# Kernel optimization log

Hardware: AMD Instinct MI355X
Metric: run time of the kernel (lower is better)

The kernel has to match this reference:

```python
import jax, jax.numpy as jnp
import numpy as np

B, NMAX, T, FIN, H, K, OUT = 64, 256, 16, 3, 32, 8, 64
N = B * NMAX            # 16384 total nodes
EPG = 2048              # edges per graph
E = B * EPG             # 131072 edges
EPS = 1e-15


def gcn_conv(x, src, dst, ew, W, b):
    # x: [N, T, FIN] -> [N, T, H]; GCNConv: symmetric norm with self-loops (weight 1)
    xw = jnp.einsum('ntf,fh->nth', x, W)
    loops = jnp.arange(N, dtype=src.dtype)
    src_a = jnp.concatenate([src, loops])
    dst_a = jnp.concatenate([dst, loops])
    w_a = jnp.concatenate([ew, jnp.ones((N,), ew.dtype)])
    deg = jax.ops.segment_sum(w_a, dst_a, num_segments=N)
    dinv = jnp.where(deg > 0, jax.lax.rsqrt(deg), 0.0)
    norm = dinv[src_a] * w_a * dinv[dst_a]
    out = jax.ops.segment_sum(xw[src_a] * norm[:, None, None], dst_a, num_segments=N)
    return out + b


def dense_mincut_pool(x, adj, s):
    # x [B,T,Nc,H], adj [B,Nc,Nc], s [B,Nc,Kc]  (mask is all-True: equal-size graphs)
    s = jax.nn.softmax(s, axis=-1)
    kc = s.shape[-1]
    out = jnp.einsum('bnk,btnh->btkh', s, x)
    out_adj = jnp.einsum('bnk,bnm,bml->bkl', s, adj, s)
    mincut_num = jnp.trace(out_adj, axis1=-2, axis2=-1)
    d_flat = adj.sum(-1)
    mincut_den = jnp.einsum('bnk,bn,bnk->b', s, d_flat, s)
    mincut_loss = -jnp.mean(mincut_num / mincut_den)
    ss = jnp.einsum('bnk,bnl->bkl', s, s)
    i_s = jnp.eye(kc, dtype=x.dtype)
    ss_n = jnp.linalg.norm(ss, axis=(-2, -1), keepdims=True)
    ortho_loss = jnp.mean(jnp.linalg.norm(ss / ss_n - i_s / jnp.sqrt(kc), axis=(-2, -1)))
    out_adj = out_adj * (1.0 - i_s)  # zero diagonal
    d = jnp.sqrt(out_adj.sum(-1))[:, None, :] + EPS  # [B,1,K]
    out_adj = out_adj / d / jnp.swapaxes(d, 1, 2)
    return out, out_adj, mincut_loss, ortho_loss


def dense_graph_conv(x, adj, Wrel, brel, Wroot):
    # DenseGraphConv(aggr='add'): lin_rel(adj @ x) + lin_root(x)
    agg = jnp.einsum('bnm,btmh->btnh', adj, x)
    return jnp.einsum('btnh,ho->btno', agg, Wrel) + brel + jnp.einsum('btnh,ho->btno', x, Wroot)


def _forward(pos, edge_attr, W1, b1, Wp1, bp1, Wrel2, brel2, Wroot2, Wp2, bp2,
             Wrel3, brel3, Wroot3, Wp3, bp3, Wrel4, brel4, Wroot4, edge_src, edge_dst):
    x = jax.nn.relu(gcn_conv(pos, edge_src, edge_dst, edge_attr, W1, b1))  # [N,T,H]
    # to_dense_batch (equal-size graphs => reshape) then transpose(1,2)
    xd = x.reshape(B, NMAX, T, H).transpose(0, 2, 1, 3)  # [B,T,NMAX,H]
    gb = edge_src // NMAX
    adj = jnp.zeros((B, NMAX, NMAX), jnp.float32).at[gb, edge_src % NMAX, edge_dst % NMAX].add(1.0)
    s1 = jnp.tanh((jnp.einsum('btnh,hk->btnk', xd, Wp1) + bp1).mean(1))   # [B,NMAX,8K]
    x1, adj1, mc1, o1 = dense_mincut_pool(xd, adj, s1)
    x1 = dense_graph_conv(x1, adj1, Wrel2, brel2, Wroot2)
    s2 = jnp.tanh((jnp.einsum('btnh,hk->btnk', x1, Wp2) + bp2).mean(1))   # [B,8K,4K]
    x2, adj2, mc2, o2 = dense_mincut_pool(x1, adj1, s2)
    x2 = dense_graph_conv(x2, adj2, Wrel3, brel3, Wroot3)
    s3 = jnp.tanh((jnp.einsum('btnh,hk->btnk', x2, Wp3) + bp3).mean(1))   # [B,4K,K]
    x3, adj3, mc3, o3 = dense_mincut_pool(x2, adj2, s3)
    x3 = dense_graph_conv(x3, adj3, Wrel4, brel4, Wroot4)                 # [B,T,K,OUT]
    p1 = jax.nn.softmax(s1, -1)
    p2 = jax.nn.softmax(s2, -1)
    p3 = jax.nn.softmax(s3, -1)
    agg = jnp.einsum('bnk,bkl,blm->bnm', p1, p2, p3)                       # [B,NMAX,K]
    return x3, mc1 + mc2 + mc3, o1 + o2 + o3, agg


def setup_inputs():
    key = jax.random.key(0)
    ks = jax.random.split(key, 16)
    pos = jax.random.normal(ks[0], (N, T, FIN), jnp.float32)
    gid = jnp.repeat(jnp.arange(B, dtype=jnp.int32), EPG)
    sl = jax.random.randint(ks[1], (E,), 0, NMAX, jnp.int32)
    dl = jax.random.randint(ks[2], (E,), 0, NMAX, jnp.int32)
    edge_src = gid * NMAX + sl
    edge_dst = gid * NMAX + dl
    edge_attr = jax.random.uniform(ks[3], (E,), jnp.float32)

    def lin(k, i, o):
        return jax.random.normal(k, (i, o), jnp.float32) / np.sqrt(i)

    return dict(
        pos=pos, edge_attr=edge_attr, edge_src=edge_src, edge_dst=edge_dst,
        W1=lin(ks[4], FIN, H), b1=jnp.zeros((H,), jnp.float32),
        Wp1=lin(ks[5], H, 8 * K), bp1=jnp.zeros((8 * K,), jnp.float32),
        Wrel2=lin(ks[6], H, H), brel2=jnp.zeros((H,), jnp.float32), Wroot2=lin(ks[7], H, H),
        Wp2=lin(ks[8], H, 4 * K), bp2=jnp.zeros((4 * K,), jnp.float32),
        Wrel3=lin(ks[9], H, H), brel3=jnp.zeros((H,), jnp.float32), Wroot3=lin(ks[10], H, H),
        Wp3=lin(ks[11], H, K), bp3=jnp.zeros((K,), jnp.float32),
        Wrel4=lin(ks[12], H, OUT), brel4=jnp.zeros((OUT,), jnp.float32), Wroot4=lin(ks[13], H, OUT),
    )


def reference(pos, edge_attr, edge_src, edge_dst, W1, b1, Wp1, bp1, Wrel2, brel2, Wroot2,
              Wp2, bp2, Wrel3, brel3, Wroot3, Wp3, bp3, Wrel4, brel4, Wroot4):
    return _forward(pos, edge_attr, W1, b1, Wp1, bp1, Wrel2, brel2, Wroot2, Wp2, bp2,
                    Wrel3, brel3, Wroot3, Wp3, bp3, Wrel4, brel4, Wroot4, edge_src, edge_dst)
```

## Files before the change

kernel.cpp:

```cpp
#include <hip/hip_runtime.h>
#include <math.h>

#define NB 64
#define TC 16
#define HC 32
#define NNODES 16384
#define NEDGES 131072
#define EPG 2048
#define EPSV 1e-15f

static inline int GRID(int n) { return (n + 255) / 256; }

template<int V> struct Log2 { static constexpr int v = 1 + Log2<V/2>::v; };
template<> struct Log2<1> { static constexpr int v = 0; };

__device__ inline float blk_sum256(float v, float* rbuf) {
    for (int o = 32; o > 0; o >>= 1) v += __shfl_xor(v, o);
    __syncthreads();
    if ((threadIdx.x & 63) == 0) rbuf[threadIdx.x >> 6] = v;
    __syncthreads();
    return rbuf[0] + rbuf[1] + rbuf[2] + rbuf[3];
}

__device__ inline float blk_sum512(float v, float* rbuf) {
    for (int o = 32; o > 0; o >>= 1) v += __shfl_xor(v, o);
    __syncthreads();
    if ((threadIdx.x & 63) == 0) rbuf[threadIdx.x >> 6] = v;
    __syncthreads();
    float s = 0.f;
#pragma unroll
    for (int i = 0; i < 8; ++i) s += rbuf[i];
    return s;
}

__global__ __launch_bounds__(256) void k_front(
        const int* __restrict__ esrc, const int* __restrict__ edst,
        const float* __restrict__ ea, const float* __restrict__ pos,
        const float* __restrict__ W1, const float* __restrict__ b1,
        const float* __restrict__ Wp1, const float* __restrict__ bp1,
        float* __restrict__ z, float* __restrict__ dinv_g,
        float* __restrict__ p1, float* __restrict__ mc) {
    __shared__ float L[9280];
    float* dinvs = L;
    float* as_   = L + 256;
    float* bs    = L + 1408;
    float* s1    = L + 256;
    float* zs    = L + 2944;
    float* poss  = L + 4480;
    float* xm    = L + 6016;
    float* wp    = L + 7040;
    float* W1s   = L + 9088;
    float* b1s   = L + 9184;
    float* bp1s  = L + 9216;
    int bid = blockIdx.x;
    int b = (bid & 7) * 8 + (bid >> 6);
    int dtile = ((bid >> 3) & 7) * 32;
    int tid = threadIdx.x;
    if (bid == 0 && tid < 2) mc[tid] = 0.f;
    for (int i = tid; i < 512; i += 256) ((float4*)wp)[i] = ((const float4*)Wp1)[i];
    if (tid < 96) W1s[tid] = W1[tid];
    if (tid < 32) b1s[tid] = b1[tid];
    if (tid < 64) bp1s[tid] = bp1[tid];
    for (int i = tid; i < 384; i += 256)
        ((float4*)poss)[i] = ((const float4*)(pos + ((size_t)b * 256 + dtile) * 48))[i];
    int ebase = b * EPG;
    int svr[8], dvr[8];
    float evr[8];
#pragma unroll
    for (int j = 0; j < 8; ++j) {
        int e = ebase + tid + j * 256;
        svr[j] = esrc[e] & 255;
        dvr[j] = edst[e] & 255;
        evr[j] = ea[e];
    }
    dinvs[tid] = 1.0f;
    __syncthreads();
#pragma unroll
    for (int j = 0; j < 8; ++j) atomicAdd(&dinvs[dvr[j]], evr[j]);
    __syncthreads();
    float dg = dinvs[tid];
    float dvv = (dg > 0.f) ? rsqrtf(dg) : 0.f;
    __syncthreads();
    dinvs[tid] = dvv;
    __syncthreads();
    if (dtile == 0) dinv_g[b * 256 + tid] = dinvs[tid];
    int d = tid >> 3, q = tid & 7;
    float acc[6];
#pragma unroll
    for (int j = 0; j < 6; ++j) acc[j] = 0.f;
    const float* pbase = pos + (size_t)b * 256 * 48;
    for (int s0 = 0; s0 < 256; s0 += 32) {
        for (int i = tid; i < 288; i += 256)
            ((float4*)as_)[i] = make_float4(0.f, 0.f, 0.f, 0.f);
        __syncthreads();
#pragma unroll
        for (int j = 0; j < 8; ++j) {
            int dr = dvr[j] - dtile, sc = svr[j] - s0;
            if ((unsigned)dr < 32u && (unsigned)sc < 32u)
                atomicAdd(&as_[dr * 36 + sc], evr[j]);
        }
        for (int i = tid; i < 384; i += 256) {
            int r = i / 12, c = i % 12;
            float4 v = *(const float4*)(pbase + (size_t)(s0 + r) * 48 + c * 4);
            float dd = dinvs[s0 + r];
            v.x *= dd; v.y *= dd; v.z *= dd; v.w *= dd;
            *(float4*)(bs + r * 48 + c * 4) = v;
        }
        __syncthreads();
#pragma unroll 8
        for (int sp = 0; sp < 32; ++sp) {
            float a = as_[d * 36 + sp];
            const float* bp = &bs[sp * 48 + q * 6];
#pragma unroll
            for (int j = 0; j < 6; ++j) acc[j] += a * bp[j];
        }
        __syncthreads();
    }
    float dd = dinvs[dtile + d];
    float* zr = z + (size_t)(b * 256 + dtile + d) * 48 + q * 6;
#pragma unroll
    for (int j = 0; j < 6; ++j) {
        float v = acc[j] * dd;
        zr[j] = v;
        zs[d * 48 + q * 6 + j] = v;
    }
    __syncthreads();
    for (int i = tid; i < 1536; i += 256) {
        int nn = i / 48;
        float d2 = dinvs[dtile + nn];
        d2 *= d2;
        poss[i] = zs[i] + poss[i] * d2;
    }
    __syncthreads();
    {
        int h = tid & 31, ng = tid >> 5;
        float w0 = W1s[h], w1 = W1s[32 + h], w2 = W1s[64 + h], bb = b1s[h];
#pragma unroll
        for (int j = 0; j < 4; ++j) {
            int nn = ng + 8 * j;
            float a = 0.f;
#pragma unroll
            for (int t = 0; t < 16; ++t) {
                const float* ap = &poss[nn * 48 + t * 3];
                float y = fmaxf(ap[0] * w0 + ap[1] * w1 + ap[2] * w2 + bb, 0.f);
                a += y;
            }
            xm[nn * 32 + h] = a * (1.0f / 16.0f);
        }
    }
    __syncthreads();
    for (int i = tid; i < 2048; i += 256) {
        int n = i >> 6, k = i & 63;
        float a = bp1s[k];
#pragma unroll 8
        for (int h2 = 0; h2 < 32; ++h2) a += xm[n * 32 + h2] * wp[h2 * 64 + k];
        s1[i] = tanhf(a);
    }
    __syncthreads();
    {
        int wid = tid >> 6, lane = tid & 63;
        for (int r0 = wid; r0 < 32; r0 += 4) {
            float v = s1[r0 * 64 + lane];
            float m = v;
            for (int o = 32; o > 0; o >>= 1) m = fmaxf(m, __shfl_xor(m, o));
            float e = expf(v - m);
            float s = e;
            for (int o = 32; o > 0; o >>= 1) s += __shfl_xor(s, o);
            p1[((size_t)b * 256 + dtile + r0) * 64 + lane] = e / s;
        }
    }
}

__global__ __launch_bounds__(256) void k_pool1f(
        const float* __restrict__ z, const float* __restrict__ pos,
        const float* __restrict__ dinv, const float* __restrict__ p1,
        const float* __restrict__ W1, const float* __restrict__ b1,
        float* __restrict__ X1A) {
    __shared__ __align__(16) float ps[4096];
    __shared__ __align__(16) float ys[4096];
    __shared__ float zc[384];
    __shared__ float pc[384];
    __shared__ float dv[64];
    __shared__ float W1s[96];
    __shared__ float b1s[32];
    int bid = blockIdx.x;
    int b = (bid & 7) * 8 + (bid >> 6);
    int t0 = ((bid >> 3) & 7) * 2;
    int tid = threadIdx.x;
    if (tid < 96) W1s[tid] = W1[tid];
    if (tid < 32) b1s[tid] = b1[tid];
    __syncthreads();
    int hh = tid & 31;
    float w0 = W1s[hh], w1 = W1s[32 + hh], w2 = W1s[64 + hh], bb = b1s[hh];
    int th = tid >> 7, r = tid & 127;
    int k0 = (r >> 3) * 4, h0 = (r & 7) * 4;
    float acc[4][4];
#pragma unroll
    for (int a = 0; a < 4; ++a)
#pragma unroll
        for (int c = 0; c < 4; ++c) acc[a][c] = 0.f;
    for (int n0 = 0; n0 < 256; n0 += 64) {
        for (int i = tid; i < 1024; i += 256)
            ((float4*)ps)[i] = ((const float4*)(p1 + ((size_t)b * 256 + n0) * 64))[i];
        if (tid < 192) {
            int n = tid / 3, c = tid % 3;
            size_t off = ((size_t)(b * 256 + n0 + n)) * 48 + t0 * 3 + c * 2;
            *(float2*)&zc[n * 6 + c * 2] = *(const float2*)(z + off);
            *(float2*)&pc[n * 6 + c * 2] = *(const float2*)(pos + off);
        }
        if (tid < 64) dv[tid] = dinv[b * 256 + n0 + tid];
        __syncthreads();
        int g = tid >> 5;
#pragma unroll
        for (int j = 0; j < 16; ++j) {
            int pidx = g * 16 + j;
            int t = pidx >> 6, nn = pidx & 63;
            float d2 = dv[nn] * dv[nn];
            const float* zp = &zc[nn * 6 + t * 3];
            const float* pp = &pc[nn * 6 + t * 3];
            float a0 = zp[0] + pp[0] * d2;
            float a1 = zp[1] + pp[1] * d2;
            float a2 = zp[2] + pp[2] * d2;
            ys[t * 2048 + nn * 32 + hh] = fmaxf(a0 * w0 + a1 * w1 + a2 * w2 + bb, 0.f);
        }
        __syncthreads();
#pragma unroll 4
        for (int n = 0; n < 64; ++n) {
            float4 kv4 = *(const float4*)&ps[n * 64 + k0];
            float4 xv4 = *(const float4*)&ys[th * 2048 + n * 32 + h0];
            float kv[4] = {kv4.x, kv4.y, kv4.z, kv4.w};
            float xv[4] = {xv4.x, xv4.y, xv4.z, xv4.w};
#pragma unroll
            for (int a = 0; a < 4; ++a)
#pragma unroll
                for (int c = 0; c < 4; ++c) acc[a][c] += kv[a] * xv[c];
        }
        __syncthreads();
    }
    float* ob = X1A + (((size_t)(b * 16 + t0 + th) * 64 + k0) * 32 + h0);
#pragma unroll
    for (int a = 0; a < 4; ++a) {
        float4 v = {acc[a][0], acc[a][1], acc[a][2], acc[a][3]};
        *(float4*)(ob + (size_t)a * 32) = v;
    }
}

__global__ void k_adjp2(const int* __restrict__ esrc, const int* __restrict__ edst,
                        const float* __restrict__ p, float* __restrict__ tmp,
                        float* __restrict__ dflat) {
    __shared__ __align__(16) float as_[32 * 260];
    __shared__ __align__(16) float ps[64 * 64];
    int bid = blockIdx.x;
    int b = (bid & 7) * 8 + (bid >> 6);
    int nt0 = ((bid >> 3) & 7) * 32;
    int tid = threadIdx.x;
    for (int i = tid; i < 32 * 260 / 4; i += 256)
        ((float4*)as_)[i] = make_float4(0.f, 0.f, 0.f, 0.f);
    __syncthreads();
    int ebase = b * EPG;
#pragma unroll
    for (int j = 0; j < 8; ++j) {
        int e = ebase + tid + j * 256;
        int sv = esrc[e] & 255;
        int nr = sv - nt0;
        if ((unsigned)nr < 32u)
            atomicAdd(&as_[nr * 260 + (edst[e] & 255)], 1.0f);
    }
    __syncthreads();
    int n = tid >> 3, l0 = (tid & 7) * 8;
    float acc[8];
#pragma unroll
    for (int j = 0; j < 8; ++j) acc[j] = 0.f;
    float rs = 0.f;
    for (int m0 = 0; m0 < 256; m0 += 64) {
        for (int i = tid; i < 64 * 64 / 4; i += 256)
            ((float4*)ps)[i] = ((const float4*)(p + ((size_t)b * 256 + m0) * 64))[i];
        __syncthreads();
#pragma unroll 4
        for (int m = 0; m < 64; ++m) {
            float av = as_[n * 260 + m0 + m];
            rs += av;
            float4 p0 = *(const float4*)&ps[m * 64 + l0];
            float4 p1v = *(const float4*)&ps[m * 64 + l0 + 4];
            acc[0] += av * p0.x; acc[1] += av * p0.y; acc[2] += av * p0.z; acc[3] += av * p0.w;
            acc[4] += av * p1v.x; acc[5] += av * p1v.y; acc[6] += av * p1v.z; acc[7] += av * p1v.w;
        }
        __syncthreads();
    }
#pragma unroll
    for (int j = 0; j < 8; ++j)
        tmp[((size_t)b * 256 + nt0 + n) * 64 + l0 + j] = acc[j];
    if ((tid & 7) == 0) dflat[(size_t)b * 256 + nt0 + n] = rs;
}

template<int NC, int KC, int NSPLIT, int KT, int LT>
__global__ void k_ssgp(const float* __restrict__ p, const float* __restrict__ tmp,
                       const float* __restrict__ dflat, float* __restrict__ G,
                       float* __restrict__ Gden) {
    constexpr int NCH = NC / NSPLIT;
    constexpr int LC = 2 * KC;
    constexpr int KQ = KC / 4;
    __shared__ __align__(16) float ab[NCH * LC];
    __shared__ float rbuf[4];
    int bid = blockIdx.x;
    int idx = bid >> 3;
    int b = (bid & 7) * 8 + idx / NSPLIT;
    int split = idx % NSPLIT;
    int n0 = split * NCH;
    int tid = threadIdx.x;
    const float* pb = p + ((size_t)b * NC + n0) * KC;
    const float* tb = tmp + ((size_t)b * NC + n0) * KC;
    const float* db = dflat + (size_t)b * NC + n0;
    for (int i = tid; i < NCH * KQ; i += 256) {
        int r = i / KQ, c = i % KQ;
        *(float4*)(ab + r * LC + c * 4) = ((const float4*)pb)[i];
        *(float4*)(ab + r * LC + KC + c * 4) = ((const float4*)tb)[i];
    }
    __syncthreads();
    float den = 0.f;
    for (int i = tid; i < NCH * KQ; i += 256) {
        int r = i / KQ, c = i % KQ;
        float4 v = *(const float4*)(ab + r * LC + c * 4);
        den += (v.x * v.x + v.y * v.y + v.z * v.z + v.w * v.w) * db[r];
    }
    int kt = tid >> 4, lt = tid & 15;
    int k0 = kt * KT, l0 = lt * LT;
    float acc[KT][LT];
#pragma unroll
    for (int r = 0; r < KT; ++r)
#pragma unroll
        for (int c = 0; c < LT; ++c) acc[r][c] = 0.f;
#pragma unroll 4
    for (int n = 0; n < NCH; ++n) {
        float kv[KT], lv[LT];
#pragma unroll
        for (int r = 0; r < KT; ++r) kv[r] = ab[n * LC + k0 + r];
#pragma unroll
        for (int c = 0; c < LT; ++c) lv[c] = ab[n * LC + l0 + c];
#pragma unroll
        for (int r = 0; r < KT; ++r)
#pragma unroll
            for (int c = 0; c < LT; ++c) acc[r][c] += kv[r] * lv[c];
    }
    float* Gb = G + ((size_t)split * NB + b) * (KC * LC);
#pragma unroll
    for (int r = 0; r < KT; ++r)
#pragma unroll
        for (int c = 0; c < LT; ++c)
            Gb[(k0 + r) * LC + l0 + c] = acc[r][c];
    float dt = blk_sum256(den, rbuf);
    if (tid == 0) Gden[(size_t)split * NB + b] = dt;
}

template<int KC, int NSPLIT, bool DFN>
__global__ void k_finish(const float* __restrict__ G, const float* __restrict__ Gden,
                         float* __restrict__ oadj_out, float* __restrict__ dfn_out,
                         float* __restrict__ mc_out, float* __restrict__ or_out) {
    constexpr int LK = Log2<KC>::v;
    constexpr int KCP = KC + 1;
    constexpr int LC = 2 * KC;
    __shared__ float sss[KC * KCP];
    __shared__ float oss[KC * KCP];
    __shared__ float dvv[KC];
    __shared__ float rbuf[4];
    int bid = blockIdx.x;
    int b = ((bid & 7) << 3) | (bid >> 3);
    int tid = threadIdx.x;
    for (int i = tid; i < KC * KC; i += 256) {
        int k = i >> LK, l = i & (KC - 1);
        float sv = 0.f, ov = 0.f;
#pragma unroll
        for (int s = 0; s < NSPLIT; ++s) {
            const float* Gb = G + ((size_t)s * NB + b) * KC * LC;
            sv += Gb[k * LC + l];
            ov += Gb[k * LC + KC + l];
        }
        sss[k * KCP + l] = sv;
        oss[k * KCP + l] = ov;
    }
    __syncthreads();
    float ssn2 = 0.f;
    for (int i = tid; i < KC * KC; i += 256) {
        int k = i >> LK, l = i & (KC - 1);
        float v = sss[k * KCP + l];
        ssn2 += v * v;
    }
    float num = 0.f;
    for (int k = tid; k < KC; k += 256) num += oss[k * KCP + k];
    float ssn2_t = blk_sum256(ssn2, rbuf);
    float num_t = blk_sum256(num, rbuf);
    float den_t = 0.f;
#pragma unroll
    for (int s = 0; s < NSPLIT; ++s) den_t += Gden[(size_t)s * NB + b];
    float inv = 1.0f / sqrtf(ssn2_t);
    float dk = rsqrtf((float)KC);
    float o2 = 0.f;
    for (int i = tid; i < KC * KC; i += 256) {
        int k = i >> LK, l = i & (KC - 1);
        float v = sss[k * KCP + l] * inv - ((k == l) ? dk : 0.f);
        o2 += v * v;
    }
    float o2_t = blk_sum256(o2, rbuf);
    if (tid == 0) {
        atomicAdd(mc_out, -(num_t / den_t) * (1.0f / NB));
        atomicAdd(or_out, sqrtf(o2_t) * (1.0f / NB));
    }
    if (tid < KC) {
        float rs = 0.f;
        for (int l = 0; l < KC; ++l) rs += oss[tid * KCP + l];
        rs -= oss[tid * KCP + tid];
        dvv[tid] = sqrtf(rs) + EPSV;
    }
    __syncthreads();
    for (int i = tid; i < KC * KC; i += 256) {
        int k = i >> LK, l = i & (KC - 1);
        float v = (k == l) ? 0.f : oss[k * KCP + l] / (dvv[k] * dvv[l]);
        oadj_out[(size_t)b * KC * KC + i] = v;
    }
    if (DFN && tid < KC) {
        float s = 0.f;
        for (int l = 0; l < KC; ++l)
            if (l != tid) s += oss[tid * KCP + l] / (dvv[tid] * dvv[l]);
        dfn_out[(size_t)b * KC + tid] = s;
    }
}

__global__ __launch_bounds__(512) void k_tail_a(
        const float* __restrict__ X1A, const float* __restrict__ oadj1,
        const float* __restrict__ dflat2, const float* __restrict__ p1,
        const float* __restrict__ Wrel2, const float* __restrict__ brel2,
        const float* __restrict__ Wroot2,
        const float* __restrict__ Wp2, const float* __restrict__ bp2,
        const float* __restrict__ Wrel3, const float* __restrict__ brel3,
        const float* __restrict__ Wroot3,
        const float* __restrict__ Wp3, const float* __restrict__ bp3,
        float* __restrict__ P2G, float* __restrict__ OADJ2G,
        float* __restrict__ P3G, float* __restrict__ OADJ3G,
        float* __restrict__ outagg,
        float* __restrict__ mc_out, float* __restrict__ or_out) {
    __shared__ __align__(16) float lds[16160];
    float* P2     = lds;
    float* XM2    = lds + 2304;
    float* OADJ2L = lds + 4608;
    float* P3L    = lds + 5760;
    float* OADJ3L = lds + 6016;
    float* DF3    = lds + 6080;
    float* DVV    = lds + 6112;
    float* RBUF   = lds + 6152;
    float* OADJ1s = lds + 6160;
    float* S      = lds + 10512;

    int bid = blockIdx.x;
    int b = ((bid & 7) << 3) | (bid >> 3);
    int tid = threadIdx.x;

    float* XM1A = S;
    for (int i = tid; i < 2048; i += 512) {
        float s = 0.f;
        for (int t = 0; t < 16; ++t) s += X1A[((size_t)b * 16 + t) * 2048 + i];
        XM1A[(i >> 5) * 36 + (i & 31)] = s * (1.0f / 16.0f);
    }
    for (int i = tid; i < 4096; i += 512)
        OADJ1s[(i >> 6) * 68 + (i & 63)] = oadj1[(size_t)b * 4096 + i];
    {
        float* WR = P2;
        float* WO = P2 + 1024;
        for (int i = tid; i < 1024; i += 512) { WR[i] = Wrel2[i]; WO[i] = Wroot2[i]; }
        __syncthreads();
        float* C1 = S + 2304;
        int n = tid >> 3, j0 = (tid & 7) * 4;
        float a4[4] = {0, 0, 0, 0};
        for (int m = 0; m < 64; ++m) {
            float av = OADJ1s[n * 68 + m];
            float4 xv = *(const float4*)&XM1A[m * 36 + j0];
            a4[0] += av * xv.x; a4[1] += av * xv.y; a4[2] += av * xv.z; a4[3] += av * xv.w;
        }
        __syncthreads();
#pragma unroll
        for (int j = 0; j < 4; ++j) C1[n * 36 + j0 + j] = a4[j];
        __syncthreads();
        float o4[4];
#pragma unroll
        for (int j = 0; j < 4; ++j) o4[j] = brel2[j0 + j];
        for (int h = 0; h < 32; ++h) {
            float c1v = C1[n * 36 + h];
            float xav = XM1A[n * 36 + h];
            float4 wr = *(const float4*)&WR[h * 32 + j0];
            float4 wo = *(const float4*)&WO[h * 32 + j0];
            o4[0] += c1v * wr.x + xav * wo.x;
            o4[1] += c1v * wr.y + xav * wo.y;
            o4[2] += c1v * wr.z + xav * wo.z;
            o4[3] += c1v * wr.w + xav * wo.w;
        }
        __syncthreads();
#pragma unroll
        for (int j = 0; j < 4; ++j) XM2[n * 36 + j0 + j] = o4[j];
        __syncthreads();
    }
    {
        float* S2 = S;
        float* WP2s = S + 2048;
        for (int i = tid; i < 1024; i += 512) WP2s[i] = Wp2[i];
        __syncthreads();
        for (int i = tid; i < 2048; i += 512) {
            int n = i >> 5, k = i & 31;
            float a = bp2[k];
            for (int h = 0; h < 32; ++h) a += XM2[n * 36 + h] * WP2s[h * 32 + k];
            S2[i] = tanhf(a);
        }
        __syncthreads();
        int lane = tid & 31, rr = tid >> 5;
        for (int r0 = 0; r0 < 64; r0 += 16) {
            int row = r0 + rr;
            float v = S2[row * 32 + lane];
            float m = v;
            for (int o = 16; o > 0; o >>= 1) m = fmaxf(m, __shfl_xor(m, o, 32));
            float e = expf(v - m);
            float s = e;
            for (int o = 16; o > 0; o >>= 1) s += __shfl_xor(s, o, 32);
            P2[row * 36 + lane] = e / s;
        }
        __syncthreads();
        for (int i = tid; i < 2048; i += 512)
            P2G[(size_t)b * 2048 + i] = P2[(i >> 5) * 36 + (i & 31)];
    }
    float* TMP2 = S;
    {
        int n = tid >> 3, l0 = (tid & 7) * 4;
        float a4[4] = {0, 0, 0, 0};
        for (int m = 0; m < 64; ++m) {
            float av = OADJ1s[n * 68 + m];
            float4 pv = *(const float4*)&P2[m * 36 + l0];
            a4[0] += av * pv.x; a4[1] += av * pv.y; a4[2] += av * pv.z; a4[3] += av * pv.w;
        }
        __syncthreads();
#pragma unroll
        for (int j = 0; j < 4; ++j) TMP2[n * 36 + l0 + j] = a4[j];
        __syncthreads();
    }
    {
        float* GS = S + 2304;
        float* GO = S + 3360;
        int k = tid >> 4, l0 = (tid & 15) * 2;
        float as2[2] = {0, 0}, ao2[2] = {0, 0};
        for (int n = 0; n < 64; ++n) {
            float pv = P2[n * 36 + k];
            float2 lp = *(const float2*)&P2[n * 36 + l0];
            float2 lt = *(const float2*)&TMP2[n * 36 + l0];
            as2[0] += pv * lp.x; as2[1] += pv * lp.y;
            ao2[0] += pv * lt.x; ao2[1] += pv * lt.y;
        }
        GS[k * 33 + l0] = as2[0]; GS[k * 33 + l0 + 1] = as2[1];
        GO[k * 33 + l0] = ao2[0]; GO[k * 33 + l0 + 1] = ao2[1];
        __syncthreads();
        const float* df2 = dflat2 + (size_t)b * 64;
        float den = 0.f;
        for (int i = tid; i < 2048; i += 512) {
            float pv = P2[(i >> 5) * 36 + (i & 31)];
            den += pv * pv * df2[i >> 5];
        }
        float ssn2 = 0.f;
        for (int i = tid; i < 1024; i += 512) {
            float v = GS[(i >> 5) * 33 + (i & 31)];
            ssn2 += v * v;
        }
        float num = 0.f;
        if (tid < 32) num = GO[tid * 33 + tid];
        float den_t = blk_sum512(den, RBUF);
        float ssn2_t = blk_sum512(ssn2, RBUF);
        float num_t = blk_sum512(num, RBUF);
        float inv = 1.0f / sqrtf(ssn2_t);
        float dk = rsqrtf(32.0f);
        float o2 = 0.f;
        for (int i = tid; i < 1024; i += 512) {
            int kk = i >> 5, ll = i & 31;
            float v = GS[kk * 33 + ll] * inv - ((kk == ll) ? dk : 0.f);
            o2 += v * v;
        }
        float o2_t = blk_sum512(o2, RBUF);
        if (tid == 0) {
            atomicAdd(mc_out, -(num_t / den_t) * (1.0f / NB));
            atomicAdd(or_out, sqrtf(o2_t) * (1.0f / NB));
        }
        if (tid < 32) {
            float rs = 0.f;
            for (int l = 0; l < 32; ++l) rs += GO[tid * 33 + l];
            rs -= GO[tid * 33 + tid];
            DVV[tid] = sqrtf(rs) + EPSV;
        }
        __syncthreads();
        for (int i = tid; i < 1024; i += 512) {
            int kk = i >> 5, ll = i & 31;
            float v = (kk == ll) ? 0.f : GO[kk * 33 + ll] / (DVV[kk] * DVV[ll]);
            OADJ2L[kk * 36 + ll] = v;
            OADJ2G[(size_t)b * 1024 + i] = v;
        }
        __syncthreads();
        if (tid < 32) {
            float s = 0.f;
            for (int l = 0; l < 32; ++l) s += OADJ2L[tid * 36 + l];
            DF3[tid] = s;
        }
        __syncthreads();
    }
    float* XM2A = S;
    {
        int k = tid >> 4, h0 = (tid & 15) * 2;
        float a2[2] = {0, 0};
        for (int n = 0; n < 64; ++n) {
            float pv = P2[n * 36 + k];
            float2 xv = *(const float2*)&XM2[n * 36 + h0];
            a2[0] += pv * xv.x; a2[1] += pv * xv.y;
        }
        __syncthreads();
        XM2A[k * 36 + h0] = a2[0];
        XM2A[k * 36 + h0 + 1] = a2[1];
        __syncthreads();
    }
    float* XM2B = S + 4352;
    {
        float* WREL3s = S + 1152;
        float* WROOT3s = S + 2176;
        float* C1 = S + 3200;
        for (int i = tid; i < 1024; i += 512) {
            WREL3s[i] = Wrel3[i];
            WROOT3s[i] = Wroot3[i];
        }
        __syncthreads();
        int n = tid >> 4, j0 = (tid & 15) * 2;
        float a2[2] = {0, 0};
        for (int m = 0; m < 32; ++m) {
            float av = OADJ2L[n * 36 + m];
            float2 xv = *(const float2*)&XM2A[m * 36 + j0];
            a2[0] += av * xv.x; a2[1] += av * xv.y;
        }
        __syncthreads();
        C1[n * 36 + j0] = a2[0];
        C1[n * 36 + j0 + 1] = a2[1];
        __syncthreads();
        float o2v[2];
        o2v[0] = brel3[j0]; o2v[1] = brel3[j0 + 1];
        for (int h = 0; h < 32; ++h) {
            float c1v = C1[n * 36 + h];
            float xav = XM2A[n * 36 + h];
            float2 wr = *(const float2*)&WREL3s[h * 32 + j0];
            float2 wo = *(const float2*)&WROOT3s[h * 32 + j0];
            o2v[0] += c1v * wr.x + xav * wo.x;
            o2v[1] += c1v * wr.y + xav * wo.y;
        }
        __syncthreads();
        XM2B[n * 36 + j0] = o2v[0];
        XM2B[n * 36 + j0 + 1] = o2v[1];
        __syncthreads();
    }
    {
        float* WP3s = S;
        for (int i = tid; i < 256; i += 512) WP3s[i] = Wp3[i];
        __syncthreads();
        if (tid < 256) {
            int n = tid >> 3, kk = tid & 7;
            float a = bp3[kk];
            for (int h = 0; h < 32; ++h) a += XM2B[n * 36 + h] * WP3s[h * 8 + kk];
            float v = tanhf(a);
            float m = v;
            for (int o = 4; o > 0; o >>= 1) m = fmaxf(m, __shfl_xor(m, o, 8));
            float e = expf(v - m);
            float s = e;
            for (int o = 4; o > 0; o >>= 1) s += __shfl_xor(s, o, 8);
            P3L[n * 8 + kk] = e / s;
        }
        __syncthreads();
        if (tid < 256) P3G[(size_t)b * 256 + tid] = P3L[tid];
        __syncthreads();
    }
    {
        float* TMP3 = S;
        float* GS3 = S + 256;
        float* GO3 = S + 336;
        if (tid < 256) {
            int n = tid >> 3, l = tid & 7;
            float a = 0.f;
            for (int m = 0; m < 32; ++m) a += OADJ2L[n * 36 + m] * P3L[m * 8 + l];
            TMP3[n * 8 + l] = a;
        }
        __syncthreads();
        if (tid < 64) {
            int k = tid >> 3, ll = tid & 7;
            float accs = 0.f, acco = 0.f;
            for (int nn = 0; nn < 32; ++nn) {
                float pv = P3L[nn * 8 + k];
                accs += pv * P3L[nn * 8 + ll];
                acco += pv * TMP3[nn * 8 + ll];
            }
            GS3[k * 9 + ll] = accs;
            GO3[k * 9 + ll] = acco;
        }
        __syncthreads();
        float den = 0.f;
        if (tid < 256) {
            float pv = P3L[tid];
            den = pv * pv * DF3[tid >> 3];
        }
        float ssn2 = 0.f;
        if (tid < 64) {
            float v = GS3[(tid >> 3) * 9 + (tid & 7)];
            ssn2 = v * v;
        }
        float num = 0.f;
        if (tid < 8) num = GO3[tid * 9 + tid];
        float den_t = blk_sum512(den, RBUF);
        float ssn2_t = blk_sum512(ssn2, RBUF);
        float num_t = blk_sum512(num, RBUF);
        float inv = 1.0f / sqrtf(ssn2_t);
        float dk = rsqrtf(8.0f);
        float o2 = 0.f;
        if (tid < 64) {
            int k = tid >> 3, ll = tid & 7;
            float v = GS3[k * 9 + ll] * inv - ((k == ll) ? dk : 0.f);
            o2 = v * v;
        }
        float o2_t = blk_sum512(o2, RBUF);
        if (tid == 0) {
            atomicAdd(mc_out, -(num_t / den_t) * (1.0f / NB));
            atomicAdd(or_out, sqrtf(o2_t) * (1.0f / NB));
        }
        if (tid < 8) {
            float rs = 0.f;
            for (int ll = 0; ll < 8; ++ll) rs += GO3[tid * 9 + ll];
            rs -= GO3[tid * 9 + tid];
            DVV[32 + tid] = sqrtf(rs) + EPSV;
        }
        __syncthreads();
        if (tid < 64) {
            int k = tid >> 3, ll = tid & 7;
            float v = (k == ll) ? 0.f : GO3[k * 9 + ll] / (DVV[32 + k] * DVV[32 + ll]);
            OADJ3L[tid] = v;
            OADJ3G[(size_t)b * 64 + tid] = v;
        }
        __syncthreads();
    }
    {
        float* Q = S;
        {
            int i = tid;
            if (i < 512) {
                int k = i >> 3, m = i & 7;
                float a = 0.f;
                for (int l = 0; l < 32; ++l) a += P2[k * 36 + l] * P3L[l * 8 + m];
                Q[i] = a;
            }
        }
        __syncthreads();
        int row = tid >> 1, m0 = (tid & 1) * 4;
        const float* p1r = p1 + ((size_t)b * 256 + row) * 64;
        float a4[4] = {0, 0, 0, 0};
        for (int k = 0; k < 64; ++k) {
            float pv = p1r[k];
#pragma unroll
            for (int m = 0; m < 4; ++m) a4[m] += pv * Q[k * 8 + m0 + m];
        }
#pragma unroll
        for (int m = 0; m < 4; ++m)
            outagg[((size_t)b * 256 + row) * 8 + m0 + m] = a4[m];
    }
}

__global__ __launch_bounds__(256) void k_tail_b(
        const float* __restrict__ X1A, const float* __restrict__ oadj1,
        const float* __restrict__ P2G, const float* __restrict__ OADJ2G,
        const float* __restrict__ P3G, const float* __restrict__ OADJ3G,
        const float* __restrict__ Wrel2, const float* __restrict__ brel2,
        const float* __restrict__ Wroot2,
        const float* __restrict__ Wrel3, const float* __restrict__ brel3,
        const float* __restrict__ Wroot3,
        const float* __restrict__ Wrel4, const float* __restrict__ brel4,
        const float* __restrict__ Wroot4,
        float* __restrict__ outx) {
    __shared__ float A[13408];
    float* X1AT = A;
    float* OADJ1s = A + 2304;
    float* WrelS = A + 6656;
    float* WrootS = A + 7680;
    float* C1a = A + 8704;
    float* X1B = A + 11008;
    int bid = blockIdx.x;
    int idxg = bid >> 3;
    int t = idxg & 15;
    int b = (bid & 7) * 8 + (idxg >> 4);
    int bt = b * 16 + t;
    int tid = threadIdx.x;
    for (int i = tid; i < 2048; i += 256)
        X1AT[(i >> 5) * 36 + (i & 31)] = X1A[(size_t)bt * 2048 + i];
    for (int i = tid; i < 4096; i += 256)
        OADJ1s[(i >> 6) * 68 + (i & 63)] = oadj1[(size_t)b * 4096 + i];
    for (int i = tid; i < 1024; i += 256) {
        WrelS[i] = Wrel2[i];
        WrootS[i] = Wroot2[i];
    }
    __syncthreads();
    {
        int n = tid >> 2, j0 = (tid & 3) * 8;
        float a8[8];
#pragma unroll
        for (int j = 0; j < 8; ++j) a8[j] = 0.f;
        for (int m = 0; m < 64; ++m) {
            float av = OADJ1s[n * 68 + m];
            float4 x1 = *(const float4*)&X1AT[m * 36 + j0];
            float4 x2 = *(const float4*)&X1AT[m * 36 + j0 + 4];
            a8[0] += av * x1.x; a8[1] += av * x1.y; a8[2] += av * x1.z; a8[3] += av * x1.w;
            a8[4] += av * x2.x; a8[5] += av * x2.y; a8[6] += av * x2.z; a8[7] += av * x2.w;
        }
        __syncthreads();
#pragma unroll
        for (int j = 0; j < 8; ++j) C1a[n * 36 + j0 + j] = a8[j];
        __syncthreads();
        float o8[8];
#pragma unroll
        for (int j = 0; j < 8; ++j) o8[j] = brel2[j0 + j];
        for (int h = 0; h < 32; ++h) {
            float c1v = C1a[n * 36 + h];
            float xav = X1AT[n * 36 + h];
            float4 wr1 = *(const float4*)&WrelS[h * 32 + j0];
            float4 wr2 = *(const float4*)&WrelS[h * 32 + j0 + 4];
            float4 wo1 = *(const float4*)&WrootS[h * 32 + j0];
            float4 wo2 = *(const float4*)&WrootS[h * 32 + j0 + 4];
            o8[0] += c1v * wr1.x + xav * wo1.x; o8[1] += c1v * wr1.y + xav * wo1.y;
            o8[2] += c1v * wr1.z + xav * wo1.z; o8[3] += c1v * wr1.w + xav * wo1.w;
            o8[4] += c1v * wr2.x + xav * wo2.x; o8[5] += c1v * wr2.y + xav * wo2.y;
            o8[6] += c1v * wr2.z + xav * wo2.z; o8[7] += c1v * wr2.w + xav * wo2.w;
        }
        __syncthreads();
#pragma unroll
        for (int j = 0; j < 8; ++j) X1B[n * 36 + j0 + j] = o8[j];
        __syncthreads();
    }
    float* P2s = A;
    float* X2A = A + 2304;
    for (int i = tid; i < 2048; i += 256)
        P2s[(i >> 5) * 36 + (i & 31)] = P2G[(size_t)b * 2048 + i];
    __syncthreads();
    {
        int k = tid >> 3, h0 = (tid & 7) * 4;
        float a4[4] = {0, 0, 0, 0};
        for (int n = 0; n < 64; ++n) {
            float pv = P2s[n * 36 + k];
            float4 xv = *(const float4*)&X1B[n * 36 + h0];
            a4[0] += pv * xv.x; a4[1] += pv * xv.y; a4[2] += pv * xv.z; a4[3] += pv * xv.w;
        }
        __syncthreads();
        *(float4*)&X2A[k * 36 + h0] = make_float4(a4[0], a4[1], a4[2], a4[3]);
        __syncthreads();
    }
    float* OADJ2s = A + 3456;
    float* Wrel3s = A + 4608;
    float* Wroot3s = A + 5632;
    float* C1b = A + 6656;
    float* X2B = A + 7808;
    for (int i = tid; i < 1024; i += 256) {
        OADJ2s[(i >> 5) * 36 + (i & 31)] = OADJ2G[(size_t)b * 1024 + i];
        Wrel3s[i] = Wrel3[i];
        Wroot3s[i] = Wroot3[i];
    }
    __syncthreads();
    {
        int n = tid >> 3, j0 = (tid & 7) * 4;
        float a4[4] = {0, 0, 0, 0};
        for (int m = 0; m < 32; ++m) {
            float av = OADJ2s[n * 36 + m];
            float4 xv = *(const float4*)&X2A[m * 36 + j0];
            a4[0] += av * xv.x; a4[1] += av * xv.y; a4[2] += av * xv.z; a4[3] += av * xv.w;
        }
        __syncthreads();
        *(float4*)&C1b[n * 36 + j0] = make_float4(a4[0], a4[1], a4[2], a4[3]);
        __syncthreads();
        float o4[4];
#pragma unroll
        for (int j = 0; j < 4; ++j) o4[j] = brel3[j0 + j];
        for (int h = 0; h < 32; ++h) {
            float c1v = C1b[n * 36 + h];
            float xav = X2A[n * 36 + h];
            float4 wr = *(const float4*)&Wrel3s[h * 32 + j0];
            float4 wo = *(const float4*)&Wroot3s[h * 32 + j0];
            o4[0] += c1v * wr.x + xav * wo.x;
            o4[1] += c1v * wr.y + xav * wo.y;
            o4[2] += c1v * wr.z + xav * wo.z;
            o4[3] += c1v * wr.w + xav * wo.w;
        }
        __syncthreads();
        *(float4*)&X2B[n * 36 + j0] = make_float4(o4[0], o4[1], o4[2], o4[3]);
        __syncthreads();
    }
    float* P3s = A;
    float* X3A = A + 8960;
    P3s[tid] = P3G[(size_t)b * 256 + tid];
    __syncthreads();
    {
        int k = tid >> 5, h = tid & 31;
        float a = 0.f;
        for (int n = 0; n < 32; ++n) a += P3s[n * 8 + k] * X2B[n * 36 + h];
        __syncthreads();
        X3A[k * 36 + h] = a;
        __syncthreads();
    }
    {
        float* OADJ3s = A + 256;
        float* C3 = A + 320;
        float* Wrel4s = A + 9248;
        float* Wroot4s = A + 11296;
        if (tid < 64) OADJ3s[tid] = OADJ3G[(size_t)b * 64 + tid];
        for (int i = tid; i < 2048; i += 256) {
            Wrel4s[i] = Wrel4[i];
            Wroot4s[i] = Wroot4[i];
        }
        __syncthreads();
        int n = tid >> 5, h = tid & 31;
        float a = 0.f;
#pragma unroll
        for (int m = 0; m < 8; ++m) a += OADJ3s[n * 8 + m] * X3A[m * 36 + h];
        C3[n * 36 + h] = a;
        __syncthreads();
        int o0 = (tid & 31) * 2;
        float a0 = brel4[o0], a1 = brel4[o0 + 1];
        for (int hh = 0; hh < 32; ++hh) {
            float c3v = C3[n * 36 + hh];
            float x3v = X3A[n * 36 + hh];
            a0 += c3v * Wrel4s[hh * 64 + o0] + x3v * Wroot4s[hh * 64 + o0];
            a1 += c3v * Wrel4s[hh * 64 + o0 + 1] + x3v * Wroot4s[hh * 64 + o0 + 1];
        }
        float* ob = outx + ((size_t)bt * 8 + n) * 64 + o0;
        ob[0] = a0;
        ob[1] = a1;
    }
}


extern "C" void kernel_launch(void* const* d_in, const int* in_sizes, int n_in,
                              void* d_out, int out_size, void* d_ws, size_t ws_size,
                              hipStream_t stream) {
    const float* pos    = (const float*)d_in[0];
    const float* ea     = (const float*)d_in[1];
    const int*   esrc   = (const int*)d_in[2];
    const int*   edst   = (const int*)d_in[3];
    const float* W1     = (const float*)d_in[4];
    const float* b1     = (const float*)d_in[5];
    const float* Wp1    = (const float*)d_in[6];
    const float* bp1    = (const float*)d_in[7];
    const float* Wrel2  = (const float*)d_in[8];
    const float* brel2  = (const float*)d_in[9];
    const float* Wroot2 = (const float*)d_in[10];
    const float* Wp2    = (const float*)d_in[11];
    const float* bp2    = (const float*)d_in[12];
    const float* Wrel3  = (const float*)d_in[13];
    const float* brel3  = (const float*)d_in[14];
    const float* Wroot3 = (const float*)d_in[15];
    const float* Wp3    = (const float*)d_in[16];
    const float* bp3    = (const float*)d_in[17];
    const float* Wrel4  = (const float*)d_in[18];
    const float* brel4  = (const float*)d_in[19];
    const float* Wroot4 = (const float*)d_in[20];
    float* out = (float*)d_out;

    char* w = (char*)d_ws;
    float* TMP    = (float*)(w);
    float* GBUF1  = (float*)(w + 4194304);
    float* X1A    = (float*)(w + 12582912);
    float* Z      = (float*)(w + 20971520);
    float* P1     = (float*)(w + 25165824);
    float* DINV   = (float*)(w + 29360128);
    float* DFLAT  = (float*)(w + 29425664);
    float* DFLAT2 = (float*)(w + 29491200);
    float* GDEN1  = (float*)(w + 29507584);
    float* OADJ1  = (float*)(w + 29622272);
    float* P2G    = (float*)(w + 30670848);
    float* OADJ2G = (float*)(w + 31195136);
    float* P3G    = (float*)(w + 31457280);
    float* OADJ3G = (float*)(w + 31522816);
    float* MC     = out + 524288;

    k_front<<<NB * 8, 256, 0, stream>>>(esrc, edst, ea, pos, W1, b1, Wp1, bp1,
                                        Z, DINV, P1, MC);
    k_pool1f<<<NB * 8, 256, 0, stream>>>(Z, pos, DINV, P1, W1, b1, X1A);
    k_adjp2<<<NB * 8, 256, 0, stream>>>(esrc, edst, P1, TMP, DFLAT);
    k_ssgp<256, 64, 4, 4, 8><<<NB * 4, 256, 0, stream>>>(P1, TMP, DFLAT, GBUF1, GDEN1);
    k_finish<64, 4, true><<<NB, 256, 0, stream>>>(GBUF1, GDEN1, OADJ1, DFLAT2, MC, MC + 1);
    k_tail_a<<<NB, 512, 0, stream>>>(X1A, OADJ1, DFLAT2, P1,
                                     Wrel2, brel2, Wroot2, Wp2, bp2,
                                     Wrel3, brel3, Wroot3, Wp3, bp3,
                                     P2G, OADJ2G, P3G, OADJ3G,
                                     out + 524290, MC, MC + 1);
    k_tail_b<<<NB * TC, 256, 0, stream>>>(X1A, OADJ1, P2G, OADJ2G, P3G, OADJ3G,
                                          Wrel2, brel2, Wroot2,
                                          Wrel3, brel3, Wroot3,
                                          Wrel4, brel4, Wroot4, out);
}
```

Measured before the change: 163.5 us.

## Replace dense adjacency-tile matmul in GCN front kernel with sparse edge worklist scatter

The front kernel used to build a dense 32x32 adjacency tile for each of eight source chunks and multiply it against scaled positions. It now stages half the graph's scaled positions in shared memory, collects the edges that hit this destination tile into a shared worklist, and scatters edge-weighted rows into the accumulator with shared atomics. This removes the mostly-zero dense multiply and about 16 barriers, at the cost of shared-memory atomic contention and an overflow fallback path. The Wp1 projection also now computes two outputs per thread with float2 loads, and a small index cleanup is made in a later kernel.

```diff
diff --git a/kernel.cpp b/kernel.cpp
--- a/kernel.cpp
+++ b/kernel.cpp
@@ -40,29 +40,28 @@
         const float* __restrict__ Wp1, const float* __restrict__ bp1,
         float* __restrict__ z, float* __restrict__ dinv_g,
         float* __restrict__ p1, float* __restrict__ mc) {
-    __shared__ float L[9280];
-    float* dinvs = L;
-    float* as_   = L + 256;
-    float* bs    = L + 1408;
-    float* s1    = L + 256;
-    float* zs    = L + 2944;
-    float* poss  = L + 4480;
-    float* xm    = L + 6016;
-    float* wp    = L + 7040;
-    float* W1s   = L + 9088;
-    float* b1s   = L + 9184;
-    float* bp1s  = L + 9216;
+    __shared__ float dinvs[256];
+    __shared__ __align__(16) float psc[128 * 48];
+    __shared__ __align__(16) float zs[32 * 48];
+    __shared__ int   wlA[768];
+    __shared__ float wlC[768];
+    __shared__ float xm[32 * 32];
+    __shared__ float W1s[96];
+    __shared__ float b1s[32];
+    __shared__ float bp1s[64];
+    __shared__ int cntS;
+    float* wp = psc;
+    float* s1 = psc + 2048;
+
     int bid = blockIdx.x;
     int b = (bid & 7) * 8 + (bid >> 6);
     int dtile = ((bid >> 3) & 7) * 32;
     int tid = threadIdx.x;
     if (bid == 0 && tid < 2) mc[tid] = 0.f;
-    for (int i = tid; i < 512; i += 256) ((float4*)wp)[i] = ((const float4*)Wp1)[i];
     if (tid < 96) W1s[tid] = W1[tid];
     if (tid < 32) b1s[tid] = b1[tid];
     if (tid < 64) bp1s[tid] = bp1[tid];
-    for (int i = tid; i < 384; i += 256)
-        ((float4*)poss)[i] = ((const float4*)(pos + ((size_t)b * 256 + dtile) * 48))[i];
+
     int ebase = b * EPG;
     int svr[8], dvr[8];
     float evr[8];
@@ -84,52 +83,60 @@
     dinvs[tid] = dvv;
     __syncthreads();
     if (dtile == 0) dinv_g[b * 256 + tid] = dinvs[tid];
-    int d = tid >> 3, q = tid & 7;
-    float acc[6];
-#pragma unroll
-    for (int j = 0; j < 6; ++j) acc[j] = 0.f;
-    const float* pbase = pos + (size_t)b * 256 * 48;
-    for (int s0 = 0; s0 < 256; s0 += 32) {
-        for (int i = tid; i < 288; i += 256)
-            ((float4*)as_)[i] = make_float4(0.f, 0.f, 0.f, 0.f);
+
+    for (int i = tid; i < 384; i += 256)
+        ((float4*)zs)[i] = make_float4(0.f, 0.f, 0.f, 0.f);
+
+    for (int half = 0; half < 2; ++half) {
+        int sb = half * 128;
+        __syncthreads();
+        const float4* pg = (const float4*)(pos + ((size_t)(b * 256 + sb)) * 48);
+        for (int i = tid; i < 1536; i += 256) {
+            float4 v = pg[i];
+            float dd = dinvs[sb + i / 12];
+            v.x *= dd; v.y *= dd; v.z *= dd; v.w *= dd;
+            ((float4*)psc)[i] = v;
+        }
+        if (tid == 0) cntS = 0;
         __syncthreads();
 #pragma unroll
         for (int j = 0; j < 8; ++j) {
-            int dr = dvr[j] - dtile, sc = svr[j] - s0;
-            if ((unsigned)dr < 32u && (unsigned)sc < 32u)
-                atomicAdd(&as_[dr * 36 + sc], evr[j]);
-        }
-        for (int i = tid; i < 384; i += 256) {
-            int r = i / 12, c = i % 12;
-            float4 v = *(const float4*)(pbase + (size_t)(s0 + r) * 48 + c * 4);
-            float dd = dinvs[s0 + r];
-            v.x *= dd; v.y *= dd; v.z *= dd; v.w *= dd;
-            *(float4*)(bs + r * 48 + c * 4) = v;
-        }
-        __syncthreads();
-#pragma unroll 8
-        for (int sp = 0; sp < 32; ++sp) {
-            float a = as_[d * 36 + sp];
-            const float* bp = &bs[sp * 48 + q * 6];
-#pragma unroll
-            for (int j = 0; j < 6; ++j) acc[j] += a * bp[j];
-        }
-        __syncthreads();
-    }
-    float dd = dinvs[dtile + d];
-    float* zr = z + (size_t)(b * 256 + dtile + d) * 48 + q * 6;
-#pragma unroll
-    for (int j = 0; j < 6; ++j) {
-        float v = acc[j] * dd;
-        zr[j] = v;
-        zs[d * 48 + q * 6 + j] = v;
-    }
-    __syncthreads();
-    for (int i = tid; i < 1536; i += 256) {
-        int nn = i / 48;
-        float d2 = dinvs[dtile + nn];
-        d2 *= d2;
-        poss[i] = zs[i] + poss[i] * d2;
+            int dr = dvr[j] - dtile, sc = svr[j] - sb;
+            if ((unsigned)dr < 32u && (unsigned)sc < 128u) {
+                int p = atomicAdd(&cntS, 1);
+                if (p < 768) {
+                    wlA[p] = (dr << 8) | sc;
+                    wlC[p] = evr[j];
+                } else {
+                    float c = evr[j];
+                    for (int f = 0; f < 48; ++f)
+                        atomicAdd(&zs[dr * 48 + f], c * psc[sc * 48 + f]);
+                }
+            }
+        }
+        __syncthreads();
+        int M = cntS;
+        if (M > 768) M = 768;
+        int tot = M * 48;
+        for (int idx = tid; idx < tot; idx += 256) {
+            int e = idx / 48;
+            int f = idx - e * 48;
+            int a = wlA[e];
+            int dr = a >> 8, sc = a & 255;
+            atomicAdd(&zs[dr * 48 + f], wlC[e] * psc[sc * 48 + f]);
+        }
+    }
+    __syncthreads();
+    {
+        const float* pgt = pos + ((size_t)(b * 256 + dtile)) * 48;
+        float* zgt = z + ((size_t)(b * 256 + dtile)) * 48;
+        for (int i = tid; i < 1536; i += 256) {
+            int nn = i / 48;
+            float dv = dinvs[dtile + nn];
+            float zv = zs[i] * dv;
+            zgt[i] = zv;
+            zs[i] = zv + pgt[i] * dv * dv;
+        }
     }
     __syncthreads();
     {
@@ -141,7 +148,7 @@
             float a = 0.f;
 #pragma unroll
             for (int t = 0; t < 16; ++t) {
-                const float* ap = &poss[nn * 48 + t * 3];
+                const float* ap = &zs[nn * 48 + t * 3];
                 float y = fmaxf(ap[0] * w0 + ap[1] * w1 + ap[2] * w2 + bb, 0.f);
                 a += y;
             }
@@ -149,12 +156,20 @@
         }
     }
     __syncthreads();
-    for (int i = tid; i < 2048; i += 256) {
-        int n = i >> 6, k = i & 63;
-        float a = bp1s[k];
+    for (int i = tid; i < 512; i += 256) ((float4*)wp)[i] = ((const float4*)Wp1)[i];
+    __syncthreads();
+    for (int i2 = tid; i2 < 1024; i2 += 256) {
+        int n = i2 >> 5, k2 = i2 & 31;
+        float ax = bp1s[2 * k2], ay = bp1s[2 * k2 + 1];
 #pragma unroll 8
-        for (int h2 = 0; h2 < 32; ++h2) a += xm[n * 32 + h2] * wp[h2 * 64 + k];
-        s1[i] = tanhf(a);
+        for (int h2 = 0; h2 < 32; ++h2) {
+            float xmv = xm[n * 32 + h2];
+            float2 w = *(const float2*)&wp[h2 * 64 + 2 * k2];
+            ax += xmv * w.x;
+            ay += xmv * w.y;
+        }
+        s1[n * 64 + 2 * k2] = tanhf(ax);
+        s1[n * 64 + 2 * k2 + 1] = tanhf(ay);
     }
     __syncthreads();
     {
@@ -741,14 +756,11 @@
     }
     {
         float* Q = S;
-        {
-            int i = tid;
-            if (i < 512) {
-                int k = i >> 3, m = i & 7;
-                float a = 0.f;
-                for (int l = 0; l < 32; ++l) a += P2[k * 36 + l] * P3L[l * 8 + m];
-                Q[i] = a;
-            }
+        if (tid < 512) {
+            int k = tid >> 3, m = tid & 7;
+            float a = 0.f;
+            for (int l = 0; l < 32; ++l) a += P2[k * 36 + l] * P3L[l * 8 + m];
+            Q[tid] = a;
         }
         __syncthreads();
         int row = tid >> 1, m0 = (tid & 1) * 4;
```

Result: slower. 183.2 us (+12.0%).

## Use 64-row destination tiles in k_front and vectorize its inner products

Applied to the files above, without the earlier changes.

Grows the destination tile of the front kernel from 32 to 64 nodes, halving the block count, so the per-graph degree computation, edge scan and source-block loading are repeated half as many times. Each thread now accumulates 12 outputs using float4 shared-memory loads, the self-loop term is fused into the z write, and the Wp1 projection computes two outputs per thread with float2 loads. The costs are fewer blocks (256) to fill the GPU, more registers per thread, and a new shared-memory layout. The k_tail_a edit only flattens a nested scope.

```diff
diff --git a/kernel.cpp b/kernel.cpp
--- a/kernel.cpp
+++ b/kernel.cpp
@@ -40,29 +40,27 @@
         const float* __restrict__ Wp1, const float* __restrict__ bp1,
         float* __restrict__ z, float* __restrict__ dinv_g,
         float* __restrict__ p1, float* __restrict__ mc) {
-    __shared__ float L[9280];
-    float* dinvs = L;
-    float* as_   = L + 256;
-    float* bs    = L + 1408;
-    float* s1    = L + 256;
-    float* zs    = L + 2944;
-    float* poss  = L + 4480;
-    float* xm    = L + 6016;
-    float* wp    = L + 7040;
-    float* W1s   = L + 9088;
-    float* b1s   = L + 9184;
-    float* bp1s  = L + 9216;
+    __shared__ float dinvs[256];
+    __shared__ __align__(16) float GA[6912];
+    __shared__ float xm[2048];
+    __shared__ float W1s[96];
+    __shared__ float b1s[32];
+    __shared__ float bp1s[64];
+    float* as_ = GA;
+    float* bs  = GA + 2304;
+    float* zs  = GA + 3840;
+    float* s1  = GA;
+    float* wp  = GA + 4352;
+
     int bid = blockIdx.x;
-    int b = (bid & 7) * 8 + (bid >> 6);
-    int dtile = ((bid >> 3) & 7) * 32;
+    int b = (bid & 7) * 8 + (bid >> 5);
+    int dtile = ((bid >> 3) & 3) * 64;
     int tid = threadIdx.x;
     if (bid == 0 && tid < 2) mc[tid] = 0.f;
-    for (int i = tid; i < 512; i += 256) ((float4*)wp)[i] = ((const float4*)Wp1)[i];
     if (tid < 96) W1s[tid] = W1[tid];
     if (tid < 32) b1s[tid] = b1[tid];
     if (tid < 64) bp1s[tid] = bp1[tid];
-    for (int i = tid; i < 384; i += 256)
-        ((float4*)poss)[i] = ((const float4*)(pos + ((size_t)b * 256 + dtile) * 48))[i];
+
     int ebase = b * EPG;
     int svr[8], dvr[8];
     float evr[8];
@@ -84,19 +82,20 @@
     dinvs[tid] = dvv;
     __syncthreads();
     if (dtile == 0) dinv_g[b * 256 + tid] = dinvs[tid];
-    int d = tid >> 3, q = tid & 7;
-    float acc[6];
-#pragma unroll
-    for (int j = 0; j < 6; ++j) acc[j] = 0.f;
+
+    int d = tid >> 2, q = tid & 3;
+    float acc[12];
+#pragma unroll
+    for (int j = 0; j < 12; ++j) acc[j] = 0.f;
     const float* pbase = pos + (size_t)b * 256 * 48;
     for (int s0 = 0; s0 < 256; s0 += 32) {
-        for (int i = tid; i < 288; i += 256)
+        for (int i = tid; i < 576; i += 256)
             ((float4*)as_)[i] = make_float4(0.f, 0.f, 0.f, 0.f);
         __syncthreads();
 #pragma unroll
         for (int j = 0; j < 8; ++j) {
             int dr = dvr[j] - dtile, sc = svr[j] - s0;
-            if ((unsigned)dr < 32u && (unsigned)sc < 32u)
+            if ((unsigned)dr < 64u && (unsigned)sc < 32u)
                 atomicAdd(&as_[dr * 36 + sc], evr[j]);
         }
         for (int i = tid; i < 384; i += 256) {
@@ -110,38 +109,50 @@
 #pragma unroll 8
         for (int sp = 0; sp < 32; ++sp) {
             float a = as_[d * 36 + sp];
-            const float* bp = &bs[sp * 48 + q * 6];
-#pragma unroll
-            for (int j = 0; j < 6; ++j) acc[j] += a * bp[j];
-        }
-        __syncthreads();
-    }
-    float dd = dinvs[dtile + d];
-    float* zr = z + (size_t)(b * 256 + dtile + d) * 48 + q * 6;
-#pragma unroll
-    for (int j = 0; j < 6; ++j) {
-        float v = acc[j] * dd;
-        zr[j] = v;
-        zs[d * 48 + q * 6 + j] = v;
-    }
-    __syncthreads();
-    for (int i = tid; i < 1536; i += 256) {
-        int nn = i / 48;
-        float d2 = dinvs[dtile + nn];
-        d2 *= d2;
-        poss[i] = zs[i] + poss[i] * d2;
+            const float* bp = &bs[sp * 48 + q * 12];
+            float4 b0 = *(const float4*)(bp);
+            float4 b1v = *(const float4*)(bp + 4);
+            float4 b2 = *(const float4*)(bp + 8);
+            acc[0] += a * b0.x;  acc[1] += a * b0.y;  acc[2] += a * b0.z;  acc[3] += a * b0.w;
+            acc[4] += a * b1v.x; acc[5] += a * b1v.y; acc[6] += a * b1v.z; acc[7] += a * b1v.w;
+            acc[8] += a * b2.x;  acc[9] += a * b2.y;  acc[10] += a * b2.z; acc[11] += a * b2.w;
+        }
+        __syncthreads();
+    }
+    {
+        float dd = dinvs[dtile + d];
+        float d2 = dd * dd;
+        const float4* pg4 = (const float4*)(pos + ((size_t)(b * 256 + dtile + d)) * 48 + q * 12);
+        float4* zg4 = (float4*)(z + ((size_t)(b * 256 + dtile + d)) * 48 + q * 12);
+        float4* zs4 = (float4*)&zs[d * 48 + q * 12];
+#pragma unroll
+        for (int j4 = 0; j4 < 3; ++j4) {
+            float4 pv = pg4[j4];
+            float4 zv;
+            zv.x = acc[j4 * 4 + 0] * dd;
+            zv.y = acc[j4 * 4 + 1] * dd;
+            zv.z = acc[j4 * 4 + 2] * dd;
+            zv.w = acc[j4 * 4 + 3] * dd;
+            zg4[j4] = zv;
+            float4 av;
+            av.x = zv.x + pv.x * d2;
+            av.y = zv.y + pv.y * d2;
+            av.z = zv.z + pv.z * d2;
+            av.w = zv.w + pv.w * d2;
+            zs4[j4] = av;
+        }
     }
     __syncthreads();
     {
         int h = tid & 31, ng = tid >> 5;
         float w0 = W1s[h], w1 = W1s[32 + h], w2 = W1s[64 + h], bb = b1s[h];
 #pragma unroll
-        for (int j = 0; j < 4; ++j) {
-            int nn = ng + 8 * j;
+        for (int j = 0; j < 8; ++j) {
+            int nn = ng * 8 + j;
             float a = 0.f;
 #pragma unroll
             for (int t = 0; t < 16; ++t) {
-                const float* ap = &poss[nn * 48 + t * 3];
+                const float* ap = &zs[nn * 48 + t * 3];
                 float y = fmaxf(ap[0] * w0 + ap[1] * w1 + ap[2] * w2 + bb, 0.f);
                 a += y;
             }
@@ -149,17 +160,25 @@
         }
     }
     __syncthreads();
-    for (int i = tid; i < 2048; i += 256) {
-        int n = i >> 6, k = i & 63;
-        float a = bp1s[k];
+    for (int i = tid; i < 512; i += 256) ((float4*)wp)[i] = ((const float4*)Wp1)[i];
+    __syncthreads();
+    for (int i2 = tid; i2 < 2048; i2 += 256) {
+        int n = i2 >> 5, k2 = i2 & 31;
+        float ax = bp1s[2 * k2], ay = bp1s[2 * k2 + 1];
 #pragma unroll 8
-        for (int h2 = 0; h2 < 32; ++h2) a += xm[n * 32 + h2] * wp[h2 * 64 + k];
-        s1[i] = tanhf(a);
+        for (int h2 = 0; h2 < 32; ++h2) {
+            float xmv = xm[n * 32 + h2];
+            float2 w = *(const float2*)&wp[h2 * 64 + 2 * k2];
+            ax += xmv * w.x;
+            ay += xmv * w.y;
+        }
+        s1[n * 64 + 2 * k2] = tanhf(ax);
+        s1[n * 64 + 2 * k2 + 1] = tanhf(ay);
     }
     __syncthreads();
     {
         int wid = tid >> 6, lane = tid & 63;
-        for (int r0 = wid; r0 < 32; r0 += 4) {
+        for (int r0 = wid; r0 < 64; r0 += 4) {
             float v = s1[r0 * 64 + lane];
             float m = v;
             for (int o = 32; o > 0; o >>= 1) m = fmaxf(m, __shfl_xor(m, o));
@@ -741,14 +760,11 @@
     }
     {
         float* Q = S;
-        {
-            int i = tid;
-            if (i < 512) {
-                int k = i >> 3, m = i & 7;
-                float a = 0.f;
-                for (int l = 0; l < 32; ++l) a += P2[k * 36 + l] * P3L[l * 8 + m];
-                Q[i] = a;
-            }
+        if (tid < 512) {
+            int k = tid >> 3, m = tid & 7;
+            float a = 0.f;
+            for (int l = 0; l < 32; ++l) a += P2[k * 36 + l] * P3L[l * 8 + m];
+            Q[tid] = a;
         }
         __syncthreads();
         int row = tid >> 1, m0 = (tid & 1) * 4;
@@ -977,7 +993,7 @@
     float* OADJ3G = (float*)(w + 31522816);
     float* MC     = out + 524288;
 
-    k_front<<<NB * 8, 256, 0, stream>>>(esrc, edst, ea, pos, W1, b1, Wp1, bp1,
+    k_front<<<NB * 4, 256, 0, stream>>>(esrc, edst, ea, pos, W1, b1, Wp1, bp1,
                                         Z, DINV, P1, MC);
     k_pool1f<<<NB * 8, 256, 0, stream>>>(Z, pos, DINV, P1, W1, b1, X1A);
     k_adjp2<<<NB * 8, 256, 0, stream>>>(esrc, edst, P1, TMP, DFLAT);
```

Result: slower. 173.3 us (+6.0%).
